# Kernel tuning notes

Hardware: AMD Instinct MI355X
Metric: run time of the kernel (lower is better)

The kernel has to match this reference:

```python
import jax, jax.numpy as jnp
import numpy as np

FIXED_POINT = 4
LOGMAX = 7
MAX_INT8 = 127
B, H = 16384, 2048


def _clipped_add(*ts):
    r = ts[0].astype(jnp.int32)
    for t in ts[1:]:
        r = r + t.astype(jnp.int32)
    return jnp.clip(r, -MAX_INT8, MAX_INT8).astype(jnp.int8)


def _int_matmul(x, w):
    # x: (..., in) int8, w: (out, in) int8 -> (..., out) int8
    r = jnp.matmul(x.astype(jnp.int32), w.T.astype(jnp.int32))
    scale = (2 ** FIXED_POINT) * int(np.sqrt(w.shape[-1]))  # 16 * 45 = 720 for H=2048
    r = r // scale  # floor division, matches torch // on ints
    return jnp.clip(r, -MAX_INT8, MAX_INT8).astype(jnp.int8)


def setup_inputs() -> dict:
    key = jax.random.key(0)
    k_x, k_s, k_wf, k_uf, k_wh, k_uh = jax.random.split(key, 6)

    def init_w(k):
        w = jax.random.normal(k, (H, H), dtype=jnp.float32) * (2 ** FIXED_POINT)
        return jnp.clip(jnp.round(w), -MAX_INT8, MAX_INT8).astype(jnp.int8)

    x = jax.random.randint(k_x, (B, H), -MAX_INT8, MAX_INT8 + 1, dtype=jnp.int32).astype(jnp.int8)
    state = jax.random.randint(k_s, (B, H), -MAX_INT8, MAX_INT8 + 1, dtype=jnp.int32).astype(jnp.int8)
    return {
        "x": x,
        "state": state,
        "W_f": init_w(k_wf),
        "U_f": init_w(k_uf),
        "b_f": jnp.zeros((H,), dtype=jnp.int8),
        "W_h": init_w(k_wh),
        "U_h": init_w(k_uh),
        "b_h": jnp.zeros((H,), dtype=jnp.int8),
    }


def reference(x, state, W_f, U_f, b_f, W_h, U_h, b_h):
    f_t = _clipped_add(_int_matmul(x, W_f), _int_matmul(state, U_f), b_f)
    f_gate = f_t.astype(jnp.int32) + MAX_INT8  # in [0, 254]
    # note: torch `a >> LOGMAX + 1` parses as a >> (LOGMAX + 1) == >> 8 (arithmetic shift)
    gated_past = (f_gate * state.astype(jnp.int32)) >> (LOGMAX + 1)
    gated_past = jnp.clip(gated_past, -MAX_INT8, MAX_INT8).astype(jnp.int8)
    h_tilde = _clipped_add(_int_matmul(x, W_h), _int_matmul(gated_past, U_h), b_h)
    diff = h_tilde.astype(jnp.int32) - state.astype(jnp.int32)
    new_state = state.astype(jnp.int32) + ((f_gate * diff) >> (LOGMAX + 1))
    new_state = jnp.clip(new_state, -MAX_INT8, MAX_INT8).astype(jnp.int8)
    return (new_state, new_state)
```

## Files before the change

kernel.cpp:

```cpp
#include <hip/hip_runtime.h>
#include <stdint.h>

#define HH 2048
#define BB 16384
#define NK (HH / 64)
#define NBH16 (1 << 21)
#define NW16  (1 << 18)

typedef int v4i __attribute__((ext_vector_type(4)));

__device__ __forceinline__ int clip127(int v){
  v = v > 127 ? 127 : v;
  return v < -127 ? -127 : v;
}
__device__ __forceinline__ int fdiv720(int r){
  int q = r / 720;
  return q - ((r - q * 720) < 0 ? 1 : 0);
}

__device__ __forceinline__ void pack16(const int* __restrict__ src, int8_t* __restrict__ dst, int i){
  const int4* s = (const int4*)src + (size_t)i * 4;
  int4 a = s[0], b = s[1], c = s[2], d = s[3];
  int4 o;
  o.x = (a.x & 255) | ((a.y & 255) << 8) | ((a.z & 255) << 16) | (a.w << 24);
  o.y = (b.x & 255) | ((b.y & 255) << 8) | ((b.z & 255) << 16) | (b.w << 24);
  o.z = (c.x & 255) | ((c.y & 255) << 8) | ((c.z & 255) << 16) | (c.w << 24);
  o.w = (d.x & 255) | ((d.y & 255) << 8) | ((d.z & 255) << 16) | (d.w << 24);
  ((int4*)dst)[i] = o;
}

__global__ void pack_all(const int* __restrict__ x,  const int* __restrict__ st,
                         const int* __restrict__ Wf, const int* __restrict__ Uf,
                         const int* __restrict__ Wh, const int* __restrict__ Uh,
                         int8_t* x8, int8_t* s8, int8_t* wf8, int8_t* uf8,
                         int8_t* wh8, int8_t* uh8){
  const int total = 2 * NBH16 + 4 * NW16;
  const int stride = gridDim.x * blockDim.x;
  for (int u = blockIdx.x * blockDim.x + threadIdx.x; u < total; u += stride){
    if (u < NBH16)            pack16(x,  x8,  u);
    else if (u < 2 * NBH16)   pack16(st, s8,  u - NBH16);
    else {
      const int v = u - 2 * NBH16;
      const int w = v >> 18;
      const int i = v & (NW16 - 1);
      if      (w == 0) pack16(Wf, wf8, i);
      else if (w == 1) pack16(Uf, uf8, i);
      else if (w == 2) pack16(Wh, wh8, i);
      else             pack16(Uh, uh8, i);
    }
  }
}

__global__ void dup_out(const int* __restrict__ src, int* __restrict__ dst, int n4){
  int stride = gridDim.x * blockDim.x;
  for (int i = blockIdx.x * blockDim.x + threadIdx.x; i < n4; i += stride)
    ((int4*)dst)[i] = ((const int4*)src)[i];
}

template<int PHASE>
__global__ __launch_bounds__(256, 2)
void gemm_dual(const int8_t* __restrict__ A1, const int8_t* __restrict__ A2,
               const int8_t* __restrict__ B1, const int8_t* __restrict__ B2,
               const int* __restrict__ bias,
               const int8_t* __restrict__ state8,
               int* fbuf, int8_t* __restrict__ g8out, int* __restrict__ out2)
{
  __shared__ __align__(16) int8_t lds[2 * 32768];
  const int tid  = threadIdx.x;
  const int lane = tid & 63;
  const int wave = tid >> 6;
  const int wrow = wave >> 1, wcol = wave & 1;

  const int bid = blockIdx.x;
  const int j   = bid >> 3;
  const int rowbase = (j >> 1) * 128;
  const int colbase = ((bid & 7) * 2 + (j & 1)) * 128;

  v4i accA[4][4], accB[4][4];
  const v4i vzero = {0, 0, 0, 0};
#pragma unroll
  for (int m = 0; m < 4; m++)
#pragma unroll
    for (int n = 0; n < 4; n++){ accA[m][n] = vzero; accB[m][n] = vzero; }

  const int srow   = tid >> 2;
  const int schunk = tid & 3;
  const int chunk  = lane >> 4;
  const int rl     = lane & 15;

  auto STAGE = [&](int buf, int kk){
    const int k0 = kk * 64;
    const int bb = buf * 32768;
#pragma unroll
    for (int p = 0; p < 2; p++){
      const int row = p * 64 + srow;
      const int swc = schunk ^ ((row >> 1) & 3);
      const size_t aoff = (size_t)(rowbase + row) * HH + k0 + swc * 16;
      const size_t boff = (size_t)(colbase + row) * HH + k0 + swc * 16;
      const int ldst = bb + p * 4096 + tid * 16;
      __builtin_amdgcn_global_load_lds((const __attribute__((address_space(1))) void*)(A1 + aoff),
                                       (__attribute__((address_space(3))) void*)(lds + ldst), 16, 0, 0);
      __builtin_amdgcn_global_load_lds((const __attribute__((address_space(1))) void*)(A2 + aoff),
                                       (__attribute__((address_space(3))) void*)(lds + 8192 + ldst), 16, 0, 0);
      __builtin_amdgcn_global_load_lds((const __attribute__((address_space(1))) void*)(B1 + boff),
                                       (__attribute__((address_space(3))) void*)(lds + 16384 + ldst), 16, 0, 0);
      __builtin_amdgcn_global_load_lds((const __attribute__((address_space(1))) void*)(B2 + boff),
                                       (__attribute__((address_space(3))) void*)(lds + 24576 + ldst), 16, 0, 0);
    }
  };

  auto COMPUTE = [&](int cb){
    {
      v4i af[4], bf[4];
#pragma unroll
      for (int m = 0; m < 4; m++){
        const int row = wrow * 64 + m * 16 + rl;
        af[m] = *(const v4i*)(lds + cb + row * 64 + ((chunk ^ ((row >> 1) & 3)) << 4));
      }
#pragma unroll
      for (int n = 0; n < 4; n++){
        const int row = wcol * 64 + n * 16 + rl;
        bf[n] = *(const v4i*)(lds + cb + 16384 + row * 64 + ((chunk ^ ((row >> 1) & 3)) << 4));
      }
#pragma unroll
      for (int m = 0; m < 4; m++)
#pragma unroll
        for (int n = 0; n < 4; n++)
          accA[m][n] = __builtin_amdgcn_mfma_i32_16x16x64_i8(af[m], bf[n], accA[m][n], 0, 0, 0);
    }
    {
      v4i af[4], bf[4];
#pragma unroll
      for (int m = 0; m < 4; m++){
        const int row = wrow * 64 + m * 16 + rl;
        af[m] = *(const v4i*)(lds + cb + 8192 + row * 64 + ((chunk ^ ((row >> 1) & 3)) << 4));
      }
#pragma unroll
      for (int n = 0; n < 4; n++){
        const int row = wcol * 64 + n * 16 + rl;
        bf[n] = *(const v4i*)(lds + cb + 24576 + row * 64 + ((chunk ^ ((row >> 1) & 3)) << 4));
      }
#pragma unroll
      for (int m = 0; m < 4; m++)
#pragma unroll
        for (int n = 0; n < 4; n++)
          accB[m][n] = __builtin_amdgcn_mfma_i32_16x16x64_i8(af[m], bf[n], accB[m][n], 0, 0, 0);
    }
  };

  STAGE(0, 0);
  STAGE(1, 1);

  for (int kk = 0; kk < NK - 1; ++kk){
    __builtin_amdgcn_sched_barrier(0);
    asm volatile("s_waitcnt vmcnt(8)" ::: "memory");
    __builtin_amdgcn_s_barrier();
    COMPUTE((kk & 1) * 32768);
    __builtin_amdgcn_sched_barrier(0);
    __builtin_amdgcn_s_barrier();
    if (kk + 2 < NK) STAGE(kk & 1, kk + 2);
  }
  __builtin_amdgcn_sched_barrier(0);
  asm volatile("s_waitcnt vmcnt(0)" ::: "memory");
  __builtin_amdgcn_s_barrier();
  COMPUTE(((NK - 1) & 1) * 32768);

  const int q = lane >> 4;
#pragma unroll
  for (int m = 0; m < 4; m++){
#pragma unroll
    for (int n = 0; n < 4; n++){
      const int gcol = colbase + wcol * 64 + n * 16 + rl;
      const int bval = bias[gcol];
#pragma unroll
      for (int r = 0; r < 4; r++){
        const int grow = rowbase + wrow * 64 + m * 16 + q * 4 + r;
        const size_t idx = (size_t)grow * HH + gcol;
        const int v1 = clip127(fdiv720(accA[m][n][r]));
        const int v2 = clip127(fdiv720(accB[m][n][r]));
        const int t  = clip127(v1 + v2 + bval);
        const int st = state8[idx];
        if (PHASE == 1){
          const int fg = t + 127;
          fbuf[idx]  = fg;
          g8out[idx] = (int8_t)clip127((fg * st) >> 8);
        } else {
          const int fg = fbuf[idx];
          const int ns = clip127(st + ((fg * (t - st)) >> 8));
          fbuf[idx] = ns;
          if (out2) out2[idx] = ns;
        }
      }
    }
  }
}

extern "C" void kernel_launch(void* const* d_in, const int* in_sizes, int n_in,
                              void* d_out, int out_size, void* d_ws, size_t ws_size,
                              hipStream_t stream){
  const int* x  = (const int*)d_in[0];
  const int* st = (const int*)d_in[1];
  const int* Wf = (const int*)d_in[2];
  const int* Uf = (const int*)d_in[3];
  const int* bf = (const int*)d_in[4];
  const int* Wh = (const int*)d_in[5];
  const int* Uh = (const int*)d_in[6];
  const int* bh = (const int*)d_in[7];

  const size_t NBH = (size_t)BB * HH;
  const size_t NW  = (size_t)HH * HH;
  const size_t need = 3 * NBH + 4 * NW;

  int*    out1   = (int*)d_out;
  const bool wsp = (ws_size >= need);
  int8_t* base   = wsp ? (int8_t*)d_ws : (int8_t*)d_out + NBH * 4;
  int8_t* x8  = base;
  int8_t* s8  = x8 + NBH;
  int8_t* g8  = s8 + NBH;
  int8_t* wf8 = g8 + NBH;
  int8_t* uf8 = wf8 + NW;
  int8_t* wh8 = uf8 + NW;
  int8_t* uh8 = wh8 + NW;

  pack_all<<<2048, 256, 0, stream>>>(x, st, Wf, Uf, Wh, Uh,
                                     x8, s8, wf8, uf8, wh8, uh8);

  gemm_dual<1><<<2048, 256, 0, stream>>>(x8, s8, wf8, uf8, bf, s8, out1, g8, nullptr);
  gemm_dual<2><<<2048, 256, 0, stream>>>(x8, g8, wh8, uh8, bh, s8, out1, nullptr,
                                         wsp ? out1 + NBH : nullptr);

  if (!wsp)
    dup_out<<<2048, 256, 0, stream>>>(out1, out1 + NBH, (int)(NBH / 4));
}
```

Measured before the change: 623.7 us.

## Store forget gate as uint8, drop double buffering, simplify block mapping

Phase 1 now writes the forget gate as one byte into a workspace buffer instead of an int32 into the output, and phase 2 reads that byte back. This cuts intermediate write and read traffic. At the same time the kernel drops the two-stage LDS prefetch pipeline for a single buffer with __syncthreads around each k-step, halving LDS use. It also replaces the grouped block-to-tile mapping with a plain row-major one. Losing the load/compute overlap and the tile grouping could hurt GEMM throughput and L2 reuse.

```diff
diff --git a/kernel.cpp b/kernel.cpp
--- a/kernel.cpp
+++ b/kernel.cpp
@@ -63,18 +63,17 @@
                const int8_t* __restrict__ B1, const int8_t* __restrict__ B2,
                const int* __restrict__ bias,
                const int8_t* __restrict__ state8,
-               int* fbuf, int8_t* __restrict__ g8out, int* __restrict__ out2)
+               uint8_t* fg8, int8_t* __restrict__ g8out,
+               int* __restrict__ out1, int* __restrict__ out2)
 {
-  __shared__ __align__(16) int8_t lds[2 * 32768];
+  __shared__ __align__(16) int8_t lds[4 * 8192];
   const int tid  = threadIdx.x;
   const int lane = tid & 63;
   const int wave = tid >> 6;
   const int wrow = wave >> 1, wcol = wave & 1;
-
-  const int bid = blockIdx.x;
-  const int j   = bid >> 3;
-  const int rowbase = (j >> 1) * 128;
-  const int colbase = ((bid & 7) * 2 + (j & 1)) * 128;
+  const int bid  = blockIdx.x;
+  const int rowbase = (bid >> 4) * 128;
+  const int colbase = (bid & 15) * 128;
 
   v4i accA[4][4], accB[4][4];
   const v4i vzero = {0, 0, 0, 0};
@@ -88,16 +87,15 @@
   const int chunk  = lane >> 4;
   const int rl     = lane & 15;
 
-  auto STAGE = [&](int buf, int kk){
+  for (int kk = 0; kk < NK; ++kk){
     const int k0 = kk * 64;
-    const int bb = buf * 32768;
 #pragma unroll
     for (int p = 0; p < 2; p++){
       const int row = p * 64 + srow;
       const int swc = schunk ^ ((row >> 1) & 3);
       const size_t aoff = (size_t)(rowbase + row) * HH + k0 + swc * 16;
       const size_t boff = (size_t)(colbase + row) * HH + k0 + swc * 16;
-      const int ldst = bb + p * 4096 + tid * 16;
+      const int ldst = p * 4096 + tid * 16;
       __builtin_amdgcn_global_load_lds((const __attribute__((address_space(1))) void*)(A1 + aoff),
                                        (__attribute__((address_space(3))) void*)(lds + ldst), 16, 0, 0);
       __builtin_amdgcn_global_load_lds((const __attribute__((address_space(1))) void*)(A2 + aoff),
@@ -107,20 +105,19 @@
       __builtin_amdgcn_global_load_lds((const __attribute__((address_space(1))) void*)(B2 + boff),
                                        (__attribute__((address_space(3))) void*)(lds + 24576 + ldst), 16, 0, 0);
     }
-  };
-
-  auto COMPUTE = [&](int cb){
+    __syncthreads();
+
     {
       v4i af[4], bf[4];
 #pragma unroll
       for (int m = 0; m < 4; m++){
         const int row = wrow * 64 + m * 16 + rl;
-        af[m] = *(const v4i*)(lds + cb + row * 64 + ((chunk ^ ((row >> 1) & 3)) << 4));
+        af[m] = *(const v4i*)(lds + row * 64 + ((chunk ^ ((row >> 1) & 3)) << 4));
       }
 #pragma unroll
       for (int n = 0; n < 4; n++){
         const int row = wcol * 64 + n * 16 + rl;
-        bf[n] = *(const v4i*)(lds + cb + 16384 + row * 64 + ((chunk ^ ((row >> 1) & 3)) << 4));
+        bf[n] = *(const v4i*)(lds + 16384 + row * 64 + ((chunk ^ ((row >> 1) & 3)) << 4));
       }
 #pragma unroll
       for (int m = 0; m < 4; m++)
@@ -133,12 +130,12 @@
 #pragma unroll
       for (int m = 0; m < 4; m++){
         const int row = wrow * 64 + m * 16 + rl;
-        af[m] = *(const v4i*)(lds + cb + 8192 + row * 64 + ((chunk ^ ((row >> 1) & 3)) << 4));
+        af[m] = *(const v4i*)(lds + 8192 + row * 64 + ((chunk ^ ((row >> 1) & 3)) << 4));
       }
 #pragma unroll
       for (int n = 0; n < 4; n++){
         const int row = wcol * 64 + n * 16 + rl;
-        bf[n] = *(const v4i*)(lds + cb + 24576 + row * 64 + ((chunk ^ ((row >> 1) & 3)) << 4));
+        bf[n] = *(const v4i*)(lds + 24576 + row * 64 + ((chunk ^ ((row >> 1) & 3)) << 4));
       }
 #pragma unroll
       for (int m = 0; m < 4; m++)
@@ -146,24 +143,8 @@
         for (int n = 0; n < 4; n++)
           accB[m][n] = __builtin_amdgcn_mfma_i32_16x16x64_i8(af[m], bf[n], accB[m][n], 0, 0, 0);
     }
-  };
-
-  STAGE(0, 0);
-  STAGE(1, 1);
-
-  for (int kk = 0; kk < NK - 1; ++kk){
-    __builtin_amdgcn_sched_barrier(0);
-    asm volatile("s_waitcnt vmcnt(8)" ::: "memory");
-    __builtin_amdgcn_s_barrier();
-    COMPUTE((kk & 1) * 32768);
-    __builtin_amdgcn_sched_barrier(0);
-    __builtin_amdgcn_s_barrier();
-    if (kk + 2 < NK) STAGE(kk & 1, kk + 2);
-  }
-  __builtin_amdgcn_sched_barrier(0);
-  asm volatile("s_waitcnt vmcnt(0)" ::: "memory");
-  __builtin_amdgcn_s_barrier();
-  COMPUTE(((NK - 1) & 1) * 32768);
+    __syncthreads();
+  }
 
   const int q = lane >> 4;
 #pragma unroll
@@ -182,13 +163,21 @@
         const int st = state8[idx];
         if (PHASE == 1){
           const int fg = t + 127;
-          fbuf[idx]  = fg;
+          fg8[idx]   = (uint8_t)fg;
+          g8out[idx] = (int8_t)clip127((fg * st) >> 8);
+        } else if (PHASE == 2){
+          const int fg = (int)fg8[idx];
+          const int ns = clip127(st + ((fg * (t - st)) >> 8));
+          out1[idx] = ns;
+          out2[idx] = ns;
+        } else if (PHASE == 3){
+          const int fg = t + 127;
+          out1[idx]  = fg;
           g8out[idx] = (int8_t)clip127((fg * st) >> 8);
         } else {
-          const int fg = fbuf[idx];
+          const int fg = out1[idx];
           const int ns = clip127(st + ((fg * (t - st)) >> 8));
-          fbuf[idx] = ns;
-          if (out2) out2[idx] = ns;
+          out1[idx] = ns;
         }
       }
     }
@@ -209,26 +198,40 @@
 
   const size_t NBH = (size_t)BB * HH;
   const size_t NW  = (size_t)HH * HH;
-  const size_t need = 3 * NBH + 4 * NW;
-
-  int*    out1   = (int*)d_out;
-  const bool wsp = (ws_size >= need);
-  int8_t* base   = wsp ? (int8_t*)d_ws : (int8_t*)d_out + NBH * 4;
-  int8_t* x8  = base;
-  int8_t* s8  = x8 + NBH;
-  int8_t* g8  = s8 + NBH;
-  int8_t* wf8 = g8 + NBH;
-  int8_t* uf8 = wf8 + NW;
-  int8_t* wh8 = uf8 + NW;
-  int8_t* uh8 = wh8 + NW;
-
-  pack_all<<<2048, 256, 0, stream>>>(x, st, Wf, Uf, Wh, Uh,
-                                     x8, s8, wf8, uf8, wh8, uh8);
-
-  gemm_dual<1><<<2048, 256, 0, stream>>>(x8, s8, wf8, uf8, bf, s8, out1, g8, nullptr);
-  gemm_dual<2><<<2048, 256, 0, stream>>>(x8, g8, wh8, uh8, bh, s8, out1, nullptr,
-                                         wsp ? out1 + NBH : nullptr);
-
-  if (!wsp)
+  const size_t need = 4 * NBH + 4 * NW;
+
+  int* out1 = (int*)d_out;
+
+  if (ws_size >= need){
+    int8_t*  x8  = (int8_t*)d_ws;
+    int8_t*  s8  = x8 + NBH;
+    int8_t*  g8  = s8 + NBH;
+    uint8_t* fg8 = (uint8_t*)(g8 + NBH);
+    int8_t*  wf8 = (int8_t*)fg8 + NBH;
+    int8_t*  uf8 = wf8 + NW;
+    int8_t*  wh8 = uf8 + NW;
+    int8_t*  uh8 = wh8 + NW;
+    pack_all<<<2048, 256, 0, stream>>>(x, st, Wf, Uf, Wh, Uh,
+                                       x8, s8, wf8, uf8, wh8, uh8);
+    gemm_dual<1><<<2048, 256, 0, stream>>>(x8, s8, wf8, uf8, bf, s8,
+                                           fg8, g8, nullptr, nullptr);
+    gemm_dual<2><<<2048, 256, 0, stream>>>(x8, g8, wh8, uh8, bh, s8,
+                                           fg8, nullptr, out1, out1 + NBH);
+  } else {
+    int8_t* base = (int8_t*)d_out + NBH * 4;
+    int8_t* x8  = base;
+    int8_t* s8  = x8 + NBH;
+    int8_t* g8  = s8 + NBH;
+    int8_t* wf8 = g8 + NBH;
+    int8_t* uf8 = wf8 + NW;
+    int8_t* wh8 = uf8 + NW;
+    int8_t* uh8 = wh8 + NW;
+    pack_all<<<2048, 256, 0, stream>>>(x, st, Wf, Uf, Wh, Uh,
+                                       x8, s8, wf8, uf8, wh8, uh8);
+    gemm_dual<3><<<2048, 256, 0, stream>>>(x8, s8, wf8, uf8, bf, s8,
+                                           nullptr, g8, out1, nullptr);
+    gemm_dual<4><<<2048, 256, 0, stream>>>(x8, g8, wh8, uh8, bh, s8,
+                                           nullptr, nullptr, out1, nullptr);
     dup_out<<<2048, 256, 0, stream>>>(out1, out1 + NBH, (int)(NBH / 4));
-}
+  }
+}
```

Result: faster. 580.4 us (-6.9%).
